# Performance work log

Measured on AMD Instinct MI355X. Metric: run time of the kernel, lower is better.

Reference implementation:

```python
import jax, jax.numpy as jnp
import numpy as np

NEG = -1e30  # stands in for float('-inf') masking; kept finite for safe grads


def setup_inputs() -> dict:
    key = jax.random.key(0)
    k1, k2 = jax.random.split(key)
    B, T, C = 256, 16, 2048
    return {
        "seq_features1": jax.random.normal(k1, (B, T, C), dtype=jnp.float32),
        "seq_features2": jax.random.normal(k2, (B, T, C), dtype=jnp.float32),
    }


def _cpa_dp(f1, f2):
    """Faithful translation of the CPA_learnStep DP core: similarity softmax ->
    2D cumsum -> 5D block/area tensors -> sequential max+gather recurrence."""
    B, T, C = f1.shape
    scores = jnp.einsum('bic,bjc->bij', f1, f2) / jnp.sqrt(jnp.asarray(C, f1.dtype))
    pred = jax.nn.softmax(scores, axis=-1)
    pred = jnp.cumsum(jnp.cumsum(pred, axis=-2), axis=-1)  # [B,T,T]

    idx1 = jnp.arange(T, dtype=pred.dtype) + 1.0
    denom = idx1[:, None] * idx1[None, :]                  # (i+1)*(j+1), [T,T]
    D0 = pred / denom                                      # D[:,0]

    # area[i,j,a,b] = denom[i,j] - denom[i,b] - denom[a,j] + denom[a,b]
    area = (denom[:, :, None, None] - denom[:, None, None, :]
            - denom[None, :, :, None] + denom[None, None, :, :])
    area = jnp.sqrt(jnp.maximum(area, 1.0))                # clamp_min(1).sqrt()

    # block[b,i,j,a,bb] = pred[b,i,j] - pred[b,i,bb] - pred[b,a,j] + pred[b,a,bb]
    block = (pred[:, :, :, None, None] - pred[:, :, None, None, :]
             - jnp.swapaxes(pred, 1, 2)[:, None, :, :, None]
             + pred[:, None, None, :, :])
    ar = jnp.arange(T)
    # mask where (a >= i) | (b >= j)
    mask = ((ar[None, None, :, None] >= ar[:, None, None, None]) |
            (ar[None, None, None, :] >= ar[None, :, None, None]))  # [T,T,T,T]
    block = jnp.where(mask[None], jnp.asarray(NEG, block.dtype), block) / area[None]
    blockf = block.reshape(B, T, T, T * T)                 # flatten (a,bb)

    def step(D_prev, _):
        # tmp[b,i,j,(a,bb)] = D_prev[b,a,bb] + block[b,i,j,a,bb]
        flat = D_prev.reshape(B, 1, 1, T * T) + blockf
        D_k = jnp.max(flat, axis=-1)                       # [B,T,T]
        ind = jnp.argmax(flat, axis=-1)                    # [B,T,T]
        blk = jnp.take_along_axis(blockf, ind[..., None], axis=-1)[..., 0]
        return D_k, (D_k[:, T - 1, T - 1], ind, blk)

    _, (fin_tail, D_ind, D_block) = jax.lax.scan(step, D0, None, length=T - 1)

    # final_result[b,k] = D[b,k,T-1,T-1]
    final_result = jnp.concatenate([D0[None, :, T - 1, T - 1], fin_tail], axis=0).T  # [B,T]
    loss_step = -jnp.max(final_result, axis=-1)
    step_num = jnp.argmax(final_result, axis=-1)
    return loss_step, step_num, D_ind, D_block


def reference(seq_features1, seq_features2):
    loss_step, step_num, D_ind, D_block = _cpa_dp(seq_features1, seq_features2)
    return loss_step, step_num
```

## Files before the change

### kernel.cpp

```cpp
#include <hip/hip_runtime.h>
#include <math.h>

#define TT 16
#define CC 2048
#define NEGV -1.0e30f
#define CW 256
#define NCK (CC / CW)
#define ASTR 260
#define PSTR 48
#define DSTR 48

#define KEEP(x) asm volatile("" : "+v"(x))

#define RORF(dst, src, n)                                                      \
    dst = __int_as_float(__builtin_amdgcn_update_dpp(                          \
        0, __float_as_int(src), 0x120 + (n), 0xF, 0xF, false))

__global__ __launch_bounds__(1024, 1) void cpa_kernel(
    const float* __restrict__ f1, const float* __restrict__ f2,
    float* __restrict__ out, int B)
{
    __shared__ float  As[TT * ASTR];
    __shared__ float  Bs[TT * ASTR];
    __shared__ float4 part4[256];
    __shared__ float  Pm[TT * PSTR];
    __shared__ float  Dm[2 * TT * DSTR];
    __shared__ float  fin[TT];

    const int b    = blockIdx.x;
    const int tid  = threadIdx.x;
    const int wv   = tid >> 6;
    const int lane = tid & 63;

    const int ti = wv >> 2, tj = wv & 3;
    const float* baseA = f1 + (size_t)b * TT * CC;
    const float* baseB = f2 + (size_t)b * TT * CC;

    float acc[4][4] = {};
    float4 av = *(const float4*)(baseA + wv * CC + lane * 4);
    float4 bv = *(const float4*)(baseB + wv * CC + lane * 4);

    for (int ck = 0; ck < NCK; ++ck) {
        *(float4*)&As[wv * ASTR + lane * 4] = av;
        *(float4*)&Bs[wv * ASTR + lane * 4] = bv;
        __syncthreads();
        if (ck + 1 < NCK) {
            av = *(const float4*)(baseA + wv * CC + (ck + 1) * CW + lane * 4);
            bv = *(const float4*)(baseB + wv * CC + (ck + 1) * CW + lane * 4);
        }
        float4 am[4], bn[4];
        #pragma unroll
        for (int m = 0; m < 4; ++m)
            am[m] = *(const float4*)&As[(ti * 4 + m) * ASTR + lane * 4];
        #pragma unroll
        for (int n = 0; n < 4; ++n)
            bn[n] = *(const float4*)&Bs[(tj * 4 + n) * ASTR + lane * 4];
        #pragma unroll
        for (int m = 0; m < 4; ++m) {
            #pragma unroll
            for (int n = 0; n < 4; ++n) {
                acc[m][n] = fmaf(am[m].x, bn[n].x, acc[m][n]);
                acc[m][n] = fmaf(am[m].y, bn[n].y, acc[m][n]);
                acc[m][n] = fmaf(am[m].z, bn[n].z, acc[m][n]);
                acc[m][n] = fmaf(am[m].w, bn[n].w, acc[m][n]);
            }
        }
        __syncthreads();
    }
    #pragma unroll
    for (int m = 0; m < 4; ++m) {
        #pragma unroll
        for (int n = 0; n < 4; ++n) {
            float v = acc[m][n], t;
            RORF(t, v, 1); v += t;
            RORF(t, v, 2); v += t;
            RORF(t, v, 4); v += t;
            RORF(t, v, 8); v += t;
            if ((lane & 15) == 0)
                ((float*)&part4[(ti * 4 + m) * 16 + (tj * 4 + n)])[lane >> 4] = v;
        }
    }
    __syncthreads();

    if (tid < 256) {
        const int si = tid >> 4, sj = tid & 15;
        float4 p = part4[tid];
        float s = (p.x + p.y + p.z + p.w) * (1.0f / sqrtf((float)CC));
        float mx = s;
        #pragma unroll
        for (int d = 1; d < 16; d <<= 1) mx = fmaxf(mx, __shfl_xor(mx, d));
        const float e = expf(s - mx);
        float sm = e;
        #pragma unroll
        for (int d = 1; d < 16; d <<= 1) sm += __shfl_xor(sm, d);
        Pm[si * PSTR + sj] = e / sm;
    }
    __syncthreads();

    if (tid < TT) {
        float run = 0.f;
        for (int r = 0; r < TT; ++r) { run += Pm[r * PSTR + tid]; Pm[r * PSTR + tid] = run; }
    }
    __syncthreads();
    if (tid < TT) {
        float run = 0.f;
        for (int c = 0; c < TT; ++c) { run += Pm[tid * PSTR + c]; Pm[tid * PSTR + c] = run; }
    }
    __syncthreads();

    const int i_dp = (int)((0x612073458ABC9DEFull >> (4 * wv)) & 15);
    const int ksD  = lane >> 4;
    const int j    = lane & 15;
    const float jf = (float)j;

    const float pij = Pm[i_dp * PSTR + j];
    float vA0 = Pm[(ksD +  0) * PSTR + j];
    float vA1 = Pm[(ksD +  4) * PSTR + j];
    float vA2 = Pm[(ksD +  8) * PSTR + j];
    float vA3 = Pm[(ksD + 12) * PSTR + j];
    float ca0, ca1, ca2, ca3, ra0, ra1, ra2, ra3;
    {
        int a, d1;
        a = ksD;      ca0 = -vA0 + (a < i_dp ? 0.f : NEGV); d1 = i_dp - a; if (d1 < 1) d1 = 1; ra0 = rsqrtf((float)d1);
        a = ksD + 4;  ca1 = -vA1 + (a < i_dp ? 0.f : NEGV); d1 = i_dp - a; if (d1 < 1) d1 = 1; ra1 = rsqrtf((float)d1);
        a = ksD + 8;  ca2 = -vA2 + (a < i_dp ? 0.f : NEGV); d1 = i_dp - a; if (d1 < 1) d1 = 1; ra2 = rsqrtf((float)d1);
        a = ksD + 12; ca3 = -vA3 + (a < i_dp ? 0.f : NEGV); d1 = i_dp - a; if (d1 < 1) d1 = 1; ra3 = rsqrtf((float)d1);
    }

    float qr[4][16];
    qr[0][0] = (ca0 + NEGV + vA0) * ra0; KEEP(qr[0][0]);
    qr[1][0] = (ca1 + NEGV + vA1) * ra1; KEEP(qr[1][0]);
    qr[2][0] = (ca2 + NEGV + vA2) * ra2; KEEP(qr[2][0]);
    qr[3][0] = (ca3 + NEGV + vA3) * ra3; KEEP(qr[3][0]);

#define QSTEP(n)                                                               \
    {                                                                          \
        float bbf, rIt, rAt;                                                   \
        RORF(bbf, jf, n);                                                      \
        RORF(rIt, pij, n);                                                     \
        const int bbi = (int)bbf;                                              \
        int d2 = j - bbi; if (d2 < 1) d2 = 1;                                  \
        const float rjt = rsqrtf((float)d2);                                   \
        const float cbm = pij - rIt + ((bbi < j) ? 0.0f : NEGV);               \
        RORF(rAt, vA0, n); qr[0][n] = (ca0 + cbm + rAt) * (ra0 * rjt); KEEP(qr[0][n]); \
        RORF(rAt, vA1, n); qr[1][n] = (ca1 + cbm + rAt) * (ra1 * rjt); KEEP(qr[1][n]); \
        RORF(rAt, vA2, n); qr[2][n] = (ca2 + cbm + rAt) * (ra2 * rjt); KEEP(qr[2][n]); \
        RORF(rAt, vA3, n); qr[3][n] = (ca3 + cbm + rAt) * (ra3 * rjt); KEEP(qr[3][n]); \
    }
    QSTEP(1)  QSTEP(2)  QSTEP(3)  QSTEP(4)  QSTEP(5)  QSTEP(6)  QSTEP(7)
    QSTEP(8)  QSTEP(9)  QSTEP(10) QSTEP(11) QSTEP(12) QSTEP(13) QSTEP(14) QSTEP(15)
#undef QSTEP

    const float D0 = pij / (float)((i_dp + 1) * (j + 1));
    if (ksD == 0) Dm[i_dp * DSTR + j] = D0;
    if (wv == 0 && lane == 15) fin[0] = D0;
    __syncthreads();

    const int nA = (i_dp + 3) >> 2;

#define DSTEP(A_, n, MACC)                                                     \
    { float dt_; RORF(dt_, dbase, n); MACC = fmaxf(MACC, dt_ + qr[A_][n]); }
#define AABLOCK(A_, TLO_)                                                      \
    if (A_ >= (TLO_) && A_ < nA) {                                             \
        const float dbase = Dold[(ksD + A_ * 4) * DSTR + j];                   \
        m0 = fmaxf(m0, dbase + qr[A_][0]);                                     \
        DSTEP(A_, 1, m1)  DSTEP(A_, 2, m2)  DSTEP(A_, 3, m3)  DSTEP(A_, 4, m0) \
        DSTEP(A_, 5, m1)  DSTEP(A_, 6, m2)  DSTEP(A_, 7, m3)  DSTEP(A_, 8, m0) \
        DSTEP(A_, 9, m1)  DSTEP(A_, 10, m2) DSTEP(A_, 11, m3) DSTEP(A_, 12, m0)\
        DSTEP(A_, 13, m1) DSTEP(A_, 14, m2) DSTEP(A_, 15, m3)                  \
    }

    #pragma unroll
    for (int k = 1; k < TT; ++k) {
        const float* Dold = Dm + ((k - 1) & 1) * (TT * DSTR);
        float*       Dnew = Dm + (k & 1)       * (TT * DSTR);
        if (i_dp >= k) {
            const int tlo = (k - 1) >> 2;
            float m0 = -3.0e38f, m1 = -3.0e38f, m2 = -3.0e38f, m3 = -3.0e38f;
            AABLOCK(0, tlo)
            AABLOCK(1, tlo)
            AABLOCK(2, tlo)
            AABLOCK(3, tlo)
            float mm = fmaxf(fmaxf(m0, m1), fmaxf(m2, m3));
            mm = fmaxf(mm, __shfl_xor(mm, 16));
            mm = fmaxf(mm, __shfl_xor(mm, 32));
            if (ksD == 0) Dnew[i_dp * DSTR + j] = mm;
            if (wv == 0 && lane == 15) fin[k] = mm;
        } else if (ksD == 0) {
            Dnew[i_dp * DSTR + j] = -3.0e38f;
        }
        __syncthreads();
    }
#undef AABLOCK
#undef DSTEP

    if (tid == 0) {
        float best = fin[0];
        int   idx  = 0;
        #pragma unroll
        for (int k = 1; k < TT; ++k) {
            if (fin[k] > best) { best = fin[k]; idx = k; }
        }
        out[b]     = -best;
        out[B + b] = (float)idx;
    }
}

extern "C" void kernel_launch(void* const* d_in, const int* in_sizes, int n_in,
                              void* d_out, int out_size, void* d_ws, size_t ws_size,
                              hipStream_t stream)
{
    const float* f1 = (const float*)d_in[0];
    const float* f2 = (const float*)d_in[1];
    float* out = (float*)d_out;
    const int B = in_sizes[0] / (TT * CC);
    hipLaunchKernelGGL(cpa_kernel, dim3(B), dim3(1024), 0, stream, f1, f2, out, B);
}
```

Measured before the change: 30.50 us.

## Deepen global prefetch, double-buffer LDS tiles, parallelize the 2D cumsum

The kernel now preloads six chunks of f1/f2 into registers and double-buffers the LDS staging tiles, which drops the trailing barrier in each chunk iteration and keeps more global loads in flight. The two serial 16-thread cumsum passes are replaced by 256-thread passes where each thread sums its own prefix, using new padded scratch arrays. The cost is more registers for the prefetch buffers, more LDS, and redundant adds in the prefix sums.

Result: slower. 63.74 us (+109.0%).

```diff
diff --git a/kernel.cpp b/kernel.cpp
--- a/kernel.cpp
+++ b/kernel.cpp
@@ -7,6 +7,8 @@
 #define CW 256
 #define NCK (CC / CW)
 #define ASTR 260
+#define BUFE (TT * ASTR)
+#define SSTR 17
 #define PSTR 48
 #define DSTR 48
 
@@ -20,9 +22,11 @@
     const float* __restrict__ f1, const float* __restrict__ f2,
     float* __restrict__ out, int B)
 {
-    __shared__ float  As[TT * ASTR];
-    __shared__ float  Bs[TT * ASTR];
+    __shared__ float  As[2 * BUFE];
+    __shared__ float  Bs[2 * BUFE];
     __shared__ float4 part4[256];
+    __shared__ float  Ps[TT * SSTR];
+    __shared__ float  Pq[TT * SSTR];
     __shared__ float  Pm[TT * PSTR];
     __shared__ float  Dm[2 * TT * DSTR];
     __shared__ float  fin[TT];
@@ -36,25 +40,32 @@
     const float* baseA = f1 + (size_t)b * TT * CC;
     const float* baseB = f2 + (size_t)b * TT * CC;
 
+    float4 avp[6], bvp[6];
+    #pragma unroll
+    for (int p = 0; p < 6; ++p) {
+        avp[p] = *(const float4*)(baseA + wv * CC + p * CW + lane * 4);
+        bvp[p] = *(const float4*)(baseB + wv * CC + p * CW + lane * 4);
+    }
+
     float acc[4][4] = {};
-    float4 av = *(const float4*)(baseA + wv * CC + lane * 4);
-    float4 bv = *(const float4*)(baseB + wv * CC + lane * 4);
-
+    #pragma unroll
     for (int ck = 0; ck < NCK; ++ck) {
-        *(float4*)&As[wv * ASTR + lane * 4] = av;
-        *(float4*)&Bs[wv * ASTR + lane * 4] = bv;
+        float* Ab = As + (ck & 1) * BUFE;
+        float* Bb = Bs + (ck & 1) * BUFE;
+        *(float4*)&Ab[wv * ASTR + lane * 4] = avp[ck % 6];
+        *(float4*)&Bb[wv * ASTR + lane * 4] = bvp[ck % 6];
+        if (ck + 6 < NCK) {
+            avp[ck % 6] = *(const float4*)(baseA + wv * CC + (ck + 6) * CW + lane * 4);
+            bvp[ck % 6] = *(const float4*)(baseB + wv * CC + (ck + 6) * CW + lane * 4);
+        }
         __syncthreads();
-        if (ck + 1 < NCK) {
-            av = *(const float4*)(baseA + wv * CC + (ck + 1) * CW + lane * 4);
-            bv = *(const float4*)(baseB + wv * CC + (ck + 1) * CW + lane * 4);
-        }
         float4 am[4], bn[4];
         #pragma unroll
         for (int m = 0; m < 4; ++m)
-            am[m] = *(const float4*)&As[(ti * 4 + m) * ASTR + lane * 4];
+            am[m] = *(const float4*)&Ab[(ti * 4 + m) * ASTR + lane * 4];
         #pragma unroll
         for (int n = 0; n < 4; ++n)
-            bn[n] = *(const float4*)&Bs[(tj * 4 + n) * ASTR + lane * 4];
+            bn[n] = *(const float4*)&Bb[(tj * 4 + n) * ASTR + lane * 4];
         #pragma unroll
         for (int m = 0; m < 4; ++m) {
             #pragma unroll
@@ -65,7 +76,6 @@
                 acc[m][n] = fmaf(am[m].w, bn[n].w, acc[m][n]);
             }
         }
-        __syncthreads();
     }
     #pragma unroll
     for (int m = 0; m < 4; ++m) {
@@ -93,18 +103,26 @@
         float sm = e;
         #pragma unroll
         for (int d = 1; d < 16; d <<= 1) sm += __shfl_xor(sm, d);
-        Pm[si * PSTR + sj] = e / sm;
-    }
-    __syncthreads();
-
-    if (tid < TT) {
-        float run = 0.f;
-        for (int r = 0; r < TT; ++r) { run += Pm[r * PSTR + tid]; Pm[r * PSTR + tid] = run; }
-    }
-    __syncthreads();
-    if (tid < TT) {
-        float run = 0.f;
-        for (int c = 0; c < TT; ++c) { run += Pm[tid * PSTR + c]; Pm[tid * PSTR + c] = run; }
+        Ps[si * SSTR + sj] = e / sm;
+    }
+    __syncthreads();
+
+    if (tid < 256) {
+        const int r = tid >> 4, c = tid & 15;
+        float run = Ps[c];
+        #pragma unroll
+        for (int rr = 1; rr < TT; ++rr)
+            if (rr <= r) run += Ps[rr * SSTR + c];
+        Pq[r * SSTR + c] = run;
+    }
+    __syncthreads();
+    if (tid < 256) {
+        const int r = tid >> 4, c = tid & 15;
+        float run = Pq[r * SSTR];
+        #pragma unroll
+        for (int cc = 1; cc < TT; ++cc)
+            if (cc <= c) run += Pq[r * SSTR + cc];
+        Pm[r * PSTR + c] = run;
     }
     __syncthreads();
 
```
